# Kernel optimization log

Hardware: AMD Instinct MI355X
Metric: run time of the kernel (lower is better)

The kernel has to match this reference:

```python
import jax, jax.numpy as jnp
import numpy as np

# Config (mirrors CorrLayerDownsample(J=3, L=8, A=1, A_prime=1, M=256, N=256,
# num_channels=1, shift_mode='samec', mask_angles=4)). With samec + 1 channel,
# every pair is 'shifted' (mask index 1) and groups (j1,j2) are contiguous in
# the global moment order, so concatenation reproduces results_storage order.
J, L, A, M, N, NB = 3, 8, 1, 256, 256, 2
MASK_ANGLES = 4
RADII = (1, 2)  # dyadic shift radii (assumed form of create_masks_shift)

def _mask_positions():
    # shift mask 1: origin plus shifts along mask_angles directions at dyadic radii
    pos = {(0, 0)}
    for k in range(MASK_ANGLES):
        th = np.pi * k / MASK_ANGLES
        for r in RADII:
            pos.add((int(round(r * np.cos(th))), int(round(r * np.sin(th)))))
    return sorted(pos)

def _union_flat_idx(h, w):
    # row-major flat indices of the union shift mask at resolution (h, w),
    # matching torch boolean-mask indexing order (mask_downsample + mask_idx_map_1)
    return np.array(sorted(((dx % h) * w + (dy % w)) for dx, dy in _mask_positions()), dtype=np.int64)

UNION_IDX = [_union_flat_idx(M >> j, N >> j) for j in range(J)]
NSHIFT = len(UNION_IDX[0])

# per-(j1,j2) channel gather indices: la = A*L*c + A*l + a = l (A=1, c=0)
# loop order in compute_idx: l1 outer, l2 inner
LA1 = np.repeat(np.arange(L), L)
LA2 = np.tile(np.arange(L), L)

def _spectral_pad(xh, Mn, Nn):
    # zero-pad Fourier representation to (Mn, Nn) -- spectral upsampling
    m, n = xh.shape[-2], xh.shape[-1]
    if (m, n) == (Mn, Nn):
        return xh
    xs = jnp.fft.fftshift(xh, axes=(-2, -1))
    ph, pw = (Mn - m) // 2, (Nn - n) // 2
    pad = [(0, 0)] * (xh.ndim - 2) + [(ph, ph), (pw, pw)]
    xp = jnp.pad(xs, pad)
    return jnp.fft.ifftshift(xp, axes=(-2, -1)) * ((Mn * Nn) / (m * n))

def _forward(xpsi_0, xpsi_1, xpsi_2):
    xs = [xpsi_0, xpsi_1, xpsi_2]
    hats = [jnp.fft.fft2(x.astype(jnp.complex64)) for x in xs]  # [nb, C, h_j, w_j]
    la1 = jnp.asarray(LA1)
    la2 = jnp.asarray(LA2)
    outs = []
    for j1 in range(J):
        h, w = M >> j1, N >> j1
        uidx = jnp.asarray(UNION_IDX[j1])
        h1 = hats[j1][:, la1]  # [nb, P=L*L, h, w]
        for j2 in range(j1, J):
            h2 = hats[j2][:, la2]
            if j2 > j1:
                h2 = _spectral_pad(h2, h, w)  # upsample coarser scale to scale j1
            corr = jnp.fft.ifft2(h1 * jnp.conj(h2)).real  # cross-correlation map
            flat = corr.reshape(corr.shape[0], corr.shape[1], h * w)
            outs.append(flat[:, :, uidx])  # masked downsample: keep shift positions
    return jnp.concatenate(outs, axis=1)  # [nb, total_pairs, NSHIFT]

def setup_inputs():
    key = jax.random.key(0)
    ks = jax.random.split(key, 3)
    return {
        "xpsi_0": jax.random.normal(ks[0], (NB, A * L, M, N), dtype=jnp.float32),
        "xpsi_1": jax.random.normal(ks[1], (NB, A * L, M // 2, N // 2), dtype=jnp.float32),
        "xpsi_2": jax.random.normal(ks[2], (NB, A * L, M // 4, N // 4), dtype=jnp.float32),
    }

def reference(xpsi_0, xpsi_1, xpsi_2):
    return _forward(xpsi_0, xpsi_1, xpsi_2)
```

## Files before the change

### kernel.cpp

```cpp
#include <hip/hip_runtime.h>

#define PI_F 3.14159265358979323846f


__device__ __forceinline__ float rtab_f(int n, int m2, int t) {
  if (t == 0) return 1.0f;
  int tw = 2 * n - 1;
  float th = PI_F * (float)t / (float)n;
  int A = (t * (m2 - 1)) & tw;
  int B = (t * m2) & tw;
  float v = sinf(PI_F * (float)A / (float)n) / sinf(th) +
            cosf(PI_F * (float)B / (float)n);
  return v / (float)m2;
}

template <int NR>
__device__ __forceinline__ void phaseA256(const float* __restrict__ vch,
                                          const float* __restrict__ sRl,
                                          float* __restrict__ sh,
                                          const int (&rls)[NR], int mxg, int s,
                                          int n2, float inv, float Pv, float a,
                                          int per, int cid) {
  int bj[NR];
#pragma unroll
  for (int j = 0; j < NR; ++j) bj[j] = (mxg - 2 + rls[j]) & 255;
  float4 acc[NR];
#pragma unroll
  for (int j = 0; j < NR; ++j) acc[j] = make_float4(0.f, 0.f, 0.f, 0.f);
  const float4* vp = (const float4*)vch + cid;
  float4 va = vp[0];
  float4 vb = vp[64];
  for (int nx = 0; nx < n2; ++nx) {
    float4 vc = make_float4(0.f, 0.f, 0.f, 0.f);
    if (nx + 2 < n2) vc = vp[(size_t)(nx + 2) * 64];
    int ss = s * nx;
#pragma unroll
    for (int j = 0; j < NR; ++j) {
      float rv = sRl[(bj[j] - ss) & 255];
      acc[j].x += rv * va.x;
      acc[j].y += rv * va.y;
      acc[j].z += rv * va.z;
      acc[j].w += rv * va.w;
    }
    va = vb;
    vb = vc;
  }
  float smy[4];
#pragma unroll
  for (int j = 0; j < 4; ++j)
    smy[j] = sinf(a * (float)((4 * cid + j) & (per - 1)));
#pragma unroll
  for (int j = 0; j < NR; ++j) {
    float q = inv * sinf(a * (float)(bj[j] & (per - 1))) * Pv;
    float4 o = acc[j];
    o.x -= q * smy[0];
    o.y -= q * smy[1];
    o.z -= q * smy[2];
    o.w -= q * smy[3];
    *(float4*)&sh[rls[j] * 256 + 4 * cid] = o;
  }
}

template <int NR>
__device__ __forceinline__ void phaseA128(const float* __restrict__ vch,
                                          const float* __restrict__ sRl,
                                          float* __restrict__ sh,
                                          const int (&rls)[NR], int mxg, int n2,
                                          float inv, float Pv, int cid) {
  int bj[NR];
#pragma unroll
  for (int j = 0; j < NR; ++j) bj[j] = (mxg - 2 + rls[j]) & 127;
  float2 acc[NR];
#pragma unroll
  for (int j = 0; j < NR; ++j) acc[j] = make_float2(0.f, 0.f);
  const float2* vp = (const float2*)vch + cid;
  float2 va = vp[0];
  float2 vb = vp[64];
  for (int nx = 0; nx < n2; ++nx) {
    float2 vc = make_float2(0.f, 0.f);
    if (nx + 2 < n2) vc = vp[(size_t)(nx + 2) * 64];
    int ss = 2 * nx;
#pragma unroll
    for (int j = 0; j < NR; ++j) {
      float rv = sRl[(bj[j] - ss) & 127];
      acc[j].x += rv * va.x;
      acc[j].y += rv * va.y;
    }
    va = vb;
    vb = vc;
  }
  const float a = PI_F * 0.5f;
  float smy0 = sinf(a * (float)((2 * cid) & 3));
  float smy1 = sinf(a * (float)((2 * cid + 1) & 3));
#pragma unroll
  for (int j = 0; j < NR; ++j) {
    float q = inv * sinf(a * (float)(bj[j] & 3)) * Pv;
    float2 o = acc[j];
    o.x -= q * smy0;
    o.y -= q * smy1;
    *(float2*)&sh[rls[j] * 128 + 2 * cid] = o;
  }
}

__global__ __launch_bounds__(256) void k_front(
    const float* __restrict__ X0, const float* __restrict__ X1,
    const float* __restrict__ X2, float* __restrict__ P1p,
    float* __restrict__ P2p, float* __restrict__ V01, float* __restrict__ V02,
    float* __restrict__ V12, float* __restrict__ out) {
  __shared__ float fsm[4864];
  int bid = blockIdx.x;
  int t = threadIdx.x;
  if (bid < 192) {
    const float* X; float* P; int lg, nsp, idx0;
    if (bid < 128) { X = X1; P = P1p; lg = 7; nsp = 8; idx0 = bid; }
    else           { X = X2; P = P2p; lg = 6; nsp = 4; idx0 = bid - 128; }
    int ch = idx0 / nsp, split = idx0 % nsp;
    int n = 1 << lg;
    int total = n * n;
    int chunk = total / nsp;
    int b0 = split * chunk;
    const float* x = X + (size_t)ch * total + b0;
    float s = 0.f;
    for (int i = t; i < chunk; i += 256) {
      int idx = b0 + i;
      float v = x[i];
      s += (((idx >> lg) ^ idx) & 1) ? -v : v;
    }
#pragma unroll
    for (int off = 32; off > 0; off >>= 1) s += __shfl_down(s, off, 64);
    __shared__ float red[4];
    if ((t & 63) == 0) red[t >> 6] = s;
    __syncthreads();
    if (t == 0) P[ch * nsp + split] = red[0] + red[1] + red[2] + red[3];
    return;
  }
  if (bid < 320) {
    int idx = bid - 192;
    int ch = idx >> 3, nxg = (idx & 7) * 16;
    float* Rl = fsm;
    float* Xs = fsm + 256;
    for (int i = t; i < 256; i += 256) Rl[i] = rtab_f(256, 128, i);
    const float4* xch4 =
        (const float4*)(X1 + (size_t)ch * 16384 + (size_t)nxg * 128);
    for (int i = t; i < 512; i += 256) ((float4*)Xs)[i] = xch4[i];
    __syncthreads();
    float* vch = V01 + (size_t)ch * 128 * 256;
    for (int i = t; i < 2048; i += 256) {
      int r = i >> 7, k = i & 127;
      vch[(size_t)(nxg + r) * 256 + 2 * k] = Xs[r * 128 + k];
    }
    int cid = t & 63, wq = t >> 6;
    int m0 = 2 * cid + 1, m1 = 2 * cid + 129;
    float acc[4][2];
#pragma unroll
    for (int r = 0; r < 4; ++r) { acc[r][0] = 0.f; acc[r][1] = 0.f; }
    for (int ny = 0; ny < 128; ++ny) {
      float r0 = Rl[(m0 - 2 * ny) & 255];
      float r1 = Rl[(m1 - 2 * ny) & 255];
#pragma unroll
      for (int r = 0; r < 4; ++r) {
        float xv = Xs[(4 * wq + r) * 128 + ny];
        acc[r][0] += xv * r0;
        acc[r][1] += xv * r1;
      }
    }
#pragma unroll
    for (int r = 0; r < 4; ++r) {
      vch[(size_t)(nxg + 4 * wq + r) * 256 + m0] = acc[r][0];
      vch[(size_t)(nxg + 4 * wq + r) * 256 + m1] = acc[r][1];
    }
    return;
  }
  if (bid < 512) {
    int vbid = bid - 320;
    const float* X = X2; float* V;
    int n1, n2, s, ch, nxg, colh;
    if (vbid < 128) {
      V = V02; n1 = 256; n2 = 64; s = 4;
      ch = vbid >> 3; nxg = ((vbid >> 1) & 3) * 16; colh = vbid & 1;
    } else {
      int w = vbid - 128;
      V = V12; n1 = 128; n2 = 64; s = 2;
      ch = w >> 2; nxg = (w & 3) * 16; colh = 0;
    }
    float* Rl = fsm;
    float* Xs = fsm + 256;
    for (int i = t; i < n1; i += 256) Rl[i] = rtab_f(n1, n2, i);
    const float4* xch4 =
        (const float4*)(X + (size_t)ch * n2 * n2 + (size_t)nxg * n2);
    int nx4 = (16 * n2) >> 2;
    for (int i = t; i < nx4; i += 256) ((float4*)Xs)[i] = xch4[i];
    __syncthreads();
    int myq = (t & 63) + colh * 128;
    int nxq = t >> 6;
    int mask = n1 - 1;
    float acc[4][2];
#pragma unroll
    for (int r = 0; r < 4; ++r)
#pragma unroll
      for (int c = 0; c < 2; ++c) acc[r][c] = 0.f;
    for (int ny = 0; ny < n2; ++ny) {
      float xv[4];
#pragma unroll
      for (int r = 0; r < 4; ++r) xv[r] = Xs[(4 * nxq + r) * n2 + ny];
#pragma unroll
      for (int c = 0; c < 2; ++c) {
        float rv = Rl[(myq + 64 * c - s * ny) & mask];
#pragma unroll
        for (int r = 0; r < 4; ++r) acc[r][c] += xv[r] * rv;
      }
    }
    float* vch = V + (size_t)ch * n2 * n1;
#pragma unroll
    for (int r = 0; r < 4; ++r)
      for (int c = 0; c < 2; ++c)
        vch[(size_t)(nxg + 4 * nxq + r) * n1 + myq + 64 * c] = acc[r][c];
    return;
  }
  int lane = t & 63;
  int wv = t >> 6;
  float accC[8][7];
#pragma unroll
  for (int i = 0; i < 8; ++i)
#pragma unroll
    for (int p = 0; p < 7; ++p) accC[i][p] = 0.f;
  int w = bid - 512;
  const float* Ab; int loc, lgn1, lgc, base;
  if (w < 256)      { loc = w;       Ab = X0; lgn1 = 8; lgc = 4; base = 0;   }
  else if (w < 384) { loc = w - 256; Ab = X1; lgn1 = 7; lgc = 3; base = 192; }
  else              { loc = w - 384; Ab = X2; lgn1 = 6; lgc = 2; base = 320; }
  int n1 = 1 << lgn1;
  int mask = n1 - 1;
  int n1sq = n1 * n1;
  int chunk = loc & ((1 << lgc) - 1);
  int bl2 = loc >> lgc;
  int b = bl2 >> 3, l2 = bl2 & 7;
  const float* A1 = Ab + (size_t)(b * 8) * n1sq;
  const float* A2 = Ab + (size_t)(b * 8 + l2) * n1sq;
  int lgtpr = lgn1 - 2;
  int tpr = 1 << lgtpr;
  int rif = 256 >> lgtpr;
  int rid = t >> lgtpr;
  int cid2 = t & (tpr - 1);
  int ty = cid2 * 4;
  int tym = (ty - 4) & mask;
  for (int rr = 0; rr < 16; rr += rif) {
    int row = chunk * 16 + rr + rid;
    const float* r0 = A2 + (size_t)row * n1;
    const float* r1 = A2 + (size_t)((row - 1) & mask) * n1;
    const float* r2 = A2 + (size_t)((row - 2) & mask) * n1;
    const float* r3 = A2 + (size_t)((row + 1) & mask) * n1;
    float4 a0 = *(const float4*)(r0 + tym);
    float4 b0 = *(const float4*)(r0 + ty);
    float4 a1 = *(const float4*)(r1 + tym);
    float4 b1 = *(const float4*)(r1 + ty);
    float4 b2 = *(const float4*)(r2 + ty);
    float4 a3 = *(const float4*)(r3 + tym);
    float4 b3 = *(const float4*)(r3 + ty);
    const float* rA = A1 + (size_t)row * n1 + ty;
#pragma unroll
    for (int l1 = 0; l1 < 8; ++l1) {
      float4 xv = *(const float4*)(rA + (size_t)l1 * n1sq);
      accC[l1][0] += xv.x * b0.x + xv.y * b0.y + xv.z * b0.z + xv.w * b0.w;
      accC[l1][1] += xv.x * a0.w + xv.y * b0.x + xv.z * b0.y + xv.w * b0.z;
      accC[l1][2] += xv.x * a0.z + xv.y * a0.w + xv.z * b0.x + xv.w * b0.y;
      accC[l1][3] += xv.x * b1.x + xv.y * b1.y + xv.z * b1.z + xv.w * b1.w;
      accC[l1][4] += xv.x * a1.w + xv.y * b1.x + xv.z * b1.y + xv.w * b1.z;
      accC[l1][5] += xv.x * b2.x + xv.y * b2.y + xv.z * b2.z + xv.w * b2.w;
      accC[l1][6] += xv.x * a3.w + xv.y * b3.x + xv.z * b3.y + xv.w * b3.z;
    }
  }
  float* sh = fsm;
  float* af = &accC[0][0];
#pragma unroll
  for (int j = 0; j < 56; ++j) {
    float v = af[j];
    v += __shfl_down(v, 32, 64);
    v += __shfl_down(v, 16, 64);
    af[j] = v;
  }
  __syncthreads();
  if (lane < 16) {
    float* rowp = sh + (wv * 16 + lane) * 60;
#pragma unroll
    for (int j = 0; j < 14; ++j)
      *(float4*)&rowp[4 * j] =
          make_float4(af[4 * j], af[4 * j + 1], af[4 * j + 2], af[4 * j + 3]);
  }
  __syncthreads();
  if (t < 224) {
    int v = t >> 2, q = t & 3;
    float s2 = 0.f;
#pragma unroll
    for (int i = 0; i < 16; ++i) s2 += sh[(q * 16 + i) * 60 + v];
    s2 += __shfl_down(s2, 2, 64);
    s2 += __shfl_down(s2, 1, 64);
    if (q == 0) {
      int l1o = v / 7, p = v % 7;
      atomicAdd(&out[((size_t)b * 384 + base + l1o * 8 + l2) * 7 + p], s2);
    }
  }
}

__global__ __launch_bounds__(256) void k_main(const float* __restrict__ X0,
                                              const float* __restrict__ X1,
                                              const float* __restrict__ V01,
                                              const float* __restrict__ V02,
                                              const float* __restrict__ V12,
                                              const float* __restrict__ P1p,
                                              const float* __restrict__ P2p,
                                              float* __restrict__ out) {
  __shared__ float sRl[256];
  __shared__ float sh[4864];
  int u = blockIdx.x;
  int t = threadIdx.x;
  int lane = t & 63;
  int wv = t >> 6;

  float accC[8][7];
#pragma unroll
  for (int i = 0; i < 8; ++i)
#pragma unroll
    for (int p = 0; p < 7; ++p) accC[i][p] = 0.f;

  const float* V; const float* Pp; const float* A1b;
  int n1, n2, s, ch, chunk, nsp, lgn1, base; float inv;
  if (u < 256) {
    V = V01; Pp = P1p; nsp = 8; A1b = X0; n1 = 256; n2 = 128; s = 2;
    inv = 1.f / 16384.f; ch = u >> 4; chunk = u & 15; lgn1 = 8; base = 64;
  } else if (u < 512) {
    int w = u - 256;
    V = V02; Pp = P2p; nsp = 4; A1b = X0; n1 = 256; n2 = 64; s = 4;
    inv = 1.f / 4096.f; ch = w >> 4; chunk = w & 15; lgn1 = 8; base = 128;
  } else {
    int w = u - 512;
    V = V12; Pp = P2p; nsp = 4; A1b = X1; n1 = 128; n2 = 64; s = 2;
    inv = 1.f / 4096.f; ch = w >> 3; chunk = w & 7; lgn1 = 7; base = 256;
  }
  int mask = n1 - 1;
  for (int i = t; i < n1; i += 256) sRl[i] = rtab_f(n1, n2, i);
  __syncthreads();
  int mxg = chunk * 16;
  int b = ch >> 3, l2 = ch & 7;
  const float* vch = V + (size_t)ch * n2 * n1;
  float Pv = 0.f;
  for (int i = 0; i < nsp; ++i) Pv += Pp[ch * nsp + i];
  float a = PI_F / (float)s;
  int per = 2 * s;

  if (n1 == 256) {
    if (s == 2) {
      if (wv < 3) {
        int rls[3] = {6 * wv + 1, 6 * wv + 3, 6 * wv + 5};
        phaseA256<3>(vch, sRl, sh, rls, mxg, 2, 128, inv, Pv, a, per, lane);
      } else {
        for (int i = lane; i < 640; i += 64) {
          int rl = 2 * (i >> 6), c4 = (i & 63) * 4;
          int mx = (mxg - 2 + rl) & 255;
          *(float4*)&sh[rl * 256 + c4] =
              *(const float4*)(vch + (size_t)(mx >> 1) * 256 + c4);
        }
      }
    } else {
      if (wv == 0) {
        int rls[4] = {0, 1, 3, 4};
        phaseA256<4>(vch, sRl, sh, rls, mxg, 4, 64, inv, Pv, a, per, lane);
      } else if (wv == 1) {
        int rls[4] = {5, 7, 8, 9};
        phaseA256<4>(vch, sRl, sh, rls, mxg, 4, 64, inv, Pv, a, per, lane);
      } else if (wv == 2) {
        int rls[3] = {11, 12, 13};
        phaseA256<3>(vch, sRl, sh, rls, mxg, 4, 64, inv, Pv, a, per, lane);
      } else {
        int rls[3] = {15, 16, 17};
        phaseA256<3>(vch, sRl, sh, rls, mxg, 4, 64, inv, Pv, a, per, lane);
      }
      for (int i = t; i < 320; i += 256) {
        int rl = 2 + 4 * (i >> 6), c4 = (i & 63) * 4;
        int mx = (mxg - 2 + rl) & 255;
        *(float4*)&sh[rl * 256 + c4] =
            *(const float4*)(vch + (size_t)(mx >> 2) * 256 + c4);
      }
    }
  } else {
    if (wv < 3) {
      int rls[3] = {6 * wv + 1, 6 * wv + 3, 6 * wv + 5};
      phaseA128<3>(vch, sRl, sh, rls, mxg, 64, inv, Pv, lane);
    } else {
      for (int i = lane; i < 320; i += 64) {
        int rl = 2 * (i >> 5), c4 = (i & 31) * 4;
        int mx = (mxg - 2 + rl) & 127;
        *(float4*)&sh[rl * 128 + c4] =
            *(const float4*)(vch + (size_t)(mx >> 1) * 128 + c4);
      }
    }
  }
  __syncthreads();

  int lgtpr = lgn1 - 2;
  int tpr = 1 << lgtpr;
  int rif = 256 >> lgtpr;
  int rid = t >> lgtpr;
  int cid2 = t & (tpr - 1);
  int ty = cid2 * 4;
  int tym = (ty - 4) & mask;
  int n1sq = n1 * n1;
  const float* A1 = A1b + (size_t)(b * 8) * n1sq;
  for (int rr = 0; rr < 16; rr += rif) {
    int ri = rr + rid;
    const float* r0 = &sh[(ri + 2) * n1];
    const float* r1 = &sh[(ri + 1) * n1];
    const float* r2 = &sh[ri * n1];
    const float* r3 = &sh[(ri + 3) * n1];
    float4 a0 = *(const float4*)(r0 + tym);
    float4 b0 = *(const float4*)(r0 + ty);
    float4 a1 = *(const float4*)(r1 + tym);
    float4 b1 = *(const float4*)(r1 + ty);
    float4 b2 = *(const float4*)(r2 + ty);
    float4 a3 = *(const float4*)(r3 + tym);
    float4 b3 = *(const float4*)(r3 + ty);
    const float* rA = A1 + (size_t)(mxg + ri) * n1 + ty;
#pragma unroll
    for (int l1 = 0; l1 < 8; ++l1) {
      float4 xv = *(const float4*)(rA + (size_t)l1 * n1sq);
      accC[l1][0] += xv.x * b0.x + xv.y * b0.y + xv.z * b0.z + xv.w * b0.w;
      accC[l1][1] += xv.x * a0.w + xv.y * b0.x + xv.z * b0.y + xv.w * b0.z;
      accC[l1][2] += xv.x * a0.z + xv.y * a0.w + xv.z * b0.x + xv.w * b0.y;
      accC[l1][3] += xv.x * b1.x + xv.y * b1.y + xv.z * b1.z + xv.w * b1.w;
      accC[l1][4] += xv.x * a1.w + xv.y * b1.x + xv.z * b1.y + xv.w * b1.z;
      accC[l1][5] += xv.x * b2.x + xv.y * b2.y + xv.z * b2.z + xv.w * b2.w;
      accC[l1][6] += xv.x * a3.w + xv.y * b3.x + xv.z * b3.y + xv.w * b3.z;
    }
  }

  float* af = &accC[0][0];
#pragma unroll
  for (int j = 0; j < 56; ++j) {
    float v = af[j];
    v += __shfl_down(v, 32, 64);
    v += __shfl_down(v, 16, 64);
    af[j] = v;
  }
  __syncthreads();
  if (lane < 16) {
    float* rowp = sh + (wv * 16 + lane) * 60;
#pragma unroll
    for (int j = 0; j < 14; ++j)
      *(float4*)&rowp[4 * j] =
          make_float4(af[4 * j], af[4 * j + 1], af[4 * j + 2], af[4 * j + 3]);
  }
  __syncthreads();
  if (t < 224) {
    int v = t >> 2, q = t & 3;
    float s2 = 0.f;
#pragma unroll
    for (int i = 0; i < 16; ++i) s2 += sh[(q * 16 + i) * 60 + v];
    s2 += __shfl_down(s2, 2, 64);
    s2 += __shfl_down(s2, 1, 64);
    if (q == 0) {
      int l1o = v / 7, p = v % 7;
      atomicAdd(&out[((size_t)b * 384 + base + l1o * 8 + l2) * 7 + p], s2);
    }
  }
}

extern "C" void kernel_launch(void* const* d_in, const int* in_sizes, int n_in,
                              void* d_out, int out_size, void* d_ws, size_t ws_size,
                              hipStream_t stream) {
  const float* X0 = (const float*)d_in[0];
  const float* X1 = (const float*)d_in[1];
  const float* X2 = (const float*)d_in[2];
  float* out = (float*)d_out;
  float* ws = (float*)d_ws;

  float* V01 = ws + 2359296;
  float* V02 = ws + 2883584;
  float* V12 = ws + 3145728;
  float* P1p = ws + 3276800;
  float* P2p = ws + 3276928;

  hipMemsetAsync(d_out, 0, (size_t)out_size, stream);
  k_front<<<960, 256, 0, stream>>>(X0, X1, X2, P1p, P2p, V01, V02, V12, out);
  k_main<<<640, 256, 0, stream>>>(X0, X1, V01, V02, V12, P1p, P2p, out);
}
```

Before: 96.56 us.

## Split row chunks across twice as many blocks and precompute interpolation tables once

Both kernels now split each 16-row chunk into two 8-row halves, doubling the grid so more blocks run in parallel and each block needs a smaller shared-memory halo. The resampling table is computed in double precision in the front kernel, written to workspace, and loaded by the main kernel instead of being recomputed with transcendental calls in every block. The front kernel also reorders its block roles so the heavy correlation blocks come first. In exchange, the halo rows overlapping each chunk are rebuilt twice, and the per-block phase-A work is split unevenly across waves.

```diff
diff --git a/kernel.cpp b/kernel.cpp
--- a/kernel.cpp
+++ b/kernel.cpp
@@ -1,17 +1,14 @@
 #include <hip/hip_runtime.h>
 
+#define PI_D 3.14159265358979323846
 #define PI_F 3.14159265358979323846f
 
 
-__device__ __forceinline__ float rtab_f(int n, int m2, int t) {
+__device__ inline float rtab_val(int n, int m2, int t) {
   if (t == 0) return 1.0f;
-  int tw = 2 * n - 1;
-  float th = PI_F * (float)t / (float)n;
-  int A = (t * (m2 - 1)) & tw;
-  int B = (t * m2) & tw;
-  float v = sinf(PI_F * (float)A / (float)n) / sinf(th) +
-            cosf(PI_F * (float)B / (float)n);
-  return v / (float)m2;
+  double th = PI_D * (double)t / (double)n;
+  double v = sin(th * (double)(m2 - 1)) / sin(th) + cos(th * (double)m2);
+  return (float)(v / (double)m2);
 }
 
 template <int NR>
@@ -106,14 +103,16 @@
     const float* __restrict__ X0, const float* __restrict__ X1,
     const float* __restrict__ X2, float* __restrict__ P1p,
     float* __restrict__ P2p, float* __restrict__ V01, float* __restrict__ V02,
-    float* __restrict__ V12, float* __restrict__ out) {
-  __shared__ float fsm[4864];
+    float* __restrict__ V12, float* __restrict__ T01, float* __restrict__ T02,
+    float* __restrict__ T12, float* __restrict__ out) {
+  __shared__ float fsm[3840];
   int bid = blockIdx.x;
   int t = threadIdx.x;
-  if (bid < 192) {
+  if (bid >= 1152) {
+    int pb = bid - 1152;
     const float* X; float* P; int lg, nsp, idx0;
-    if (bid < 128) { X = X1; P = P1p; lg = 7; nsp = 8; idx0 = bid; }
-    else           { X = X2; P = P2p; lg = 6; nsp = 4; idx0 = bid - 128; }
+    if (pb < 128) { X = X1; P = P1p; lg = 7; nsp = 8; idx0 = pb; }
+    else          { X = X2; P = P2p; lg = 6; nsp = 4; idx0 = pb - 128; }
     int ch = idx0 / nsp, split = idx0 % nsp;
     int n = 1 << lg;
     int total = n * n;
@@ -134,16 +133,18 @@
     if (t == 0) P[ch * nsp + split] = red[0] + red[1] + red[2] + red[3];
     return;
   }
-  if (bid < 320) {
-    int idx = bid - 192;
+  if (bid >= 768 && bid < 896) {
+    int idx = bid - 768;
     int ch = idx >> 3, nxg = (idx & 7) * 16;
     float* Rl = fsm;
     float* Xs = fsm + 256;
-    for (int i = t; i < 256; i += 256) Rl[i] = rtab_f(256, 128, i);
+    for (int i = t; i < 256; i += 256) Rl[i] = rtab_val(256, 128, i);
     const float4* xch4 =
         (const float4*)(X1 + (size_t)ch * 16384 + (size_t)nxg * 128);
     for (int i = t; i < 512; i += 256) ((float4*)Xs)[i] = xch4[i];
     __syncthreads();
+    if (idx == 0)
+      for (int i = t; i < 256; i += 256) T01[i] = Rl[i];
     float* vch = V01 + (size_t)ch * 128 * 256;
     for (int i = t; i < 2048; i += 256) {
       int r = i >> 7, k = i & 127;
@@ -171,8 +172,8 @@
     }
     return;
   }
-  if (bid < 512) {
-    int vbid = bid - 320;
+  if (bid >= 896 && bid < 1088) {
+    int vbid = bid - 896;
     const float* X = X2; float* V;
     int n1, n2, s, ch, nxg, colh;
     if (vbid < 128) {
@@ -185,12 +186,16 @@
     }
     float* Rl = fsm;
     float* Xs = fsm + 256;
-    for (int i = t; i < n1; i += 256) Rl[i] = rtab_f(n1, n2, i);
+    for (int i = t; i < n1; i += 256) Rl[i] = rtab_val(n1, n2, i);
     const float4* xch4 =
         (const float4*)(X + (size_t)ch * n2 * n2 + (size_t)nxg * n2);
     int nx4 = (16 * n2) >> 2;
     for (int i = t; i < nx4; i += 256) ((float4*)Xs)[i] = xch4[i];
     __syncthreads();
+    if (vbid == 0)
+      for (int i = t; i < 256; i += 256) T02[i] = Rl[i];
+    if (vbid == 128)
+      for (int i = t; i < 128; i += 256) T12[i] = Rl[i];
     int myq = (t & 63) + colh * 128;
     int nxq = t >> 6;
     int mask = n1 - 1;
@@ -224,11 +229,18 @@
   for (int i = 0; i < 8; ++i)
 #pragma unroll
     for (int p = 0; p < 7; ++p) accC[i][p] = 0.f;
-  int w = bid - 512;
-  const float* Ab; int loc, lgn1, lgc, base;
-  if (w < 256)      { loc = w;       Ab = X0; lgn1 = 8; lgc = 4; base = 0;   }
-  else if (w < 384) { loc = w - 256; Ab = X1; lgn1 = 7; lgc = 3; base = 192; }
-  else              { loc = w - 384; Ab = X2; lgn1 = 6; lgc = 2; base = 320; }
+  const float* Ab; int loc, half, lgn1, lgc, base, nrows;
+  if (bid < 512) {
+    loc = bid >> 1; half = bid & 1; Ab = X0; lgn1 = 8; lgc = 4; base = 0;
+    nrows = 8;
+  } else if (bid < 768) {
+    int q = bid - 512;
+    loc = q >> 1; half = q & 1; Ab = X1; lgn1 = 7; lgc = 3; base = 192;
+    nrows = 8;
+  } else {
+    loc = bid - 1088; half = 0; Ab = X2; lgn1 = 6; lgc = 2; base = 320;
+    nrows = 16;
+  }
   int n1 = 1 << lgn1;
   int mask = n1 - 1;
   int n1sq = n1 * n1;
@@ -244,8 +256,9 @@
   int cid2 = t & (tpr - 1);
   int ty = cid2 * 4;
   int tym = (ty - 4) & mask;
-  for (int rr = 0; rr < 16; rr += rif) {
-    int row = chunk * 16 + rr + rid;
+  int row0 = chunk * 16 + half * 8;
+  for (int rr = 0; rr < nrows; rr += rif) {
+    int row = row0 + rr + rid;
     const float* r0 = A2 + (size_t)row * n1;
     const float* r1 = A2 + (size_t)((row - 1) & mask) * n1;
     const float* r2 = A2 + (size_t)((row - 2) & mask) * n1;
@@ -309,10 +322,15 @@
                                               const float* __restrict__ V12,
                                               const float* __restrict__ P1p,
                                               const float* __restrict__ P2p,
+                                              const float* __restrict__ T01,
+                                              const float* __restrict__ T02,
+                                              const float* __restrict__ T12,
                                               float* __restrict__ out) {
   __shared__ float sRl[256];
-  __shared__ float sh[4864];
-  int u = blockIdx.x;
+  __shared__ float sh[3840];
+  int up = blockIdx.x;
+  int u = up >> 1;
+  int half = up & 1;
   int t = threadIdx.x;
   int lane = t & 63;
   int wv = t >> 6;
@@ -323,24 +341,27 @@
 #pragma unroll
     for (int p = 0; p < 7; ++p) accC[i][p] = 0.f;
 
-  const float* V; const float* Pp; const float* A1b;
+  const float* V; const float* Pp; const float* A1b; const float* T;
   int n1, n2, s, ch, chunk, nsp, lgn1, base; float inv;
   if (u < 256) {
     V = V01; Pp = P1p; nsp = 8; A1b = X0; n1 = 256; n2 = 128; s = 2;
     inv = 1.f / 16384.f; ch = u >> 4; chunk = u & 15; lgn1 = 8; base = 64;
+    T = T01;
   } else if (u < 512) {
     int w = u - 256;
     V = V02; Pp = P2p; nsp = 4; A1b = X0; n1 = 256; n2 = 64; s = 4;
     inv = 1.f / 4096.f; ch = w >> 4; chunk = w & 15; lgn1 = 8; base = 128;
+    T = T02;
   } else {
     int w = u - 512;
     V = V12; Pp = P2p; nsp = 4; A1b = X1; n1 = 128; n2 = 64; s = 2;
     inv = 1.f / 4096.f; ch = w >> 3; chunk = w & 7; lgn1 = 7; base = 256;
+    T = T12;
   }
   int mask = n1 - 1;
-  for (int i = t; i < n1; i += 256) sRl[i] = rtab_f(n1, n2, i);
+  for (int i = t; i < n1; i += 256) sRl[i] = T[i];
   __syncthreads();
-  int mxg = chunk * 16;
+  int mxg = chunk * 16 + half * 8;
   int b = ch >> 3, l2 = ch & 7;
   const float* vch = V + (size_t)ch * n2 * n1;
   float Pv = 0.f;
@@ -350,11 +371,17 @@
 
   if (n1 == 256) {
     if (s == 2) {
-      if (wv < 3) {
-        int rls[3] = {6 * wv + 1, 6 * wv + 3, 6 * wv + 5};
-        phaseA256<3>(vch, sRl, sh, rls, mxg, 2, 128, inv, Pv, a, per, lane);
+      if (wv == 0) {
+        int rls[2] = {1, 3};
+        phaseA256<2>(vch, sRl, sh, rls, mxg, 2, 128, inv, Pv, a, per, lane);
+      } else if (wv == 1) {
+        int rls[2] = {5, 7};
+        phaseA256<2>(vch, sRl, sh, rls, mxg, 2, 128, inv, Pv, a, per, lane);
+      } else if (wv == 2) {
+        int rls[1] = {9};
+        phaseA256<1>(vch, sRl, sh, rls, mxg, 2, 128, inv, Pv, a, per, lane);
       } else {
-        for (int i = lane; i < 640; i += 64) {
+        for (int i = lane; i < 384; i += 64) {
           int rl = 2 * (i >> 6), c4 = (i & 63) * 4;
           int mx = (mxg - 2 + rl) & 255;
           *(float4*)&sh[rl * 256 + c4] =
@@ -363,19 +390,19 @@
       }
     } else {
       if (wv == 0) {
-        int rls[4] = {0, 1, 3, 4};
-        phaseA256<4>(vch, sRl, sh, rls, mxg, 4, 64, inv, Pv, a, per, lane);
+        int rls[2] = {0, 1};
+        phaseA256<2>(vch, sRl, sh, rls, mxg, 4, 64, inv, Pv, a, per, lane);
       } else if (wv == 1) {
-        int rls[4] = {5, 7, 8, 9};
-        phaseA256<4>(vch, sRl, sh, rls, mxg, 4, 64, inv, Pv, a, per, lane);
+        int rls[2] = {3, 4};
+        phaseA256<2>(vch, sRl, sh, rls, mxg, 4, 64, inv, Pv, a, per, lane);
       } else if (wv == 2) {
-        int rls[3] = {11, 12, 13};
-        phaseA256<3>(vch, sRl, sh, rls, mxg, 4, 64, inv, Pv, a, per, lane);
+        int rls[2] = {5, 7};
+        phaseA256<2>(vch, sRl, sh, rls, mxg, 4, 64, inv, Pv, a, per, lane);
       } else {
-        int rls[3] = {15, 16, 17};
-        phaseA256<3>(vch, sRl, sh, rls, mxg, 4, 64, inv, Pv, a, per, lane);
+        int rls[2] = {8, 9};
+        phaseA256<2>(vch, sRl, sh, rls, mxg, 4, 64, inv, Pv, a, per, lane);
       }
-      for (int i = t; i < 320; i += 256) {
+      for (int i = t; i < 192; i += 256) {
         int rl = 2 + 4 * (i >> 6), c4 = (i & 63) * 4;
         int mx = (mxg - 2 + rl) & 255;
         *(float4*)&sh[rl * 256 + c4] =
@@ -383,11 +410,17 @@
       }
     }
   } else {
-    if (wv < 3) {
-      int rls[3] = {6 * wv + 1, 6 * wv + 3, 6 * wv + 5};
-      phaseA128<3>(vch, sRl, sh, rls, mxg, 64, inv, Pv, lane);
+    if (wv == 0) {
+      int rls[2] = {1, 3};
+      phaseA128<2>(vch, sRl, sh, rls, mxg, 64, inv, Pv, lane);
+    } else if (wv == 1) {
+      int rls[2] = {5, 7};
+      phaseA128<2>(vch, sRl, sh, rls, mxg, 64, inv, Pv, lane);
+    } else if (wv == 2) {
+      int rls[1] = {9};
+      phaseA128<1>(vch, sRl, sh, rls, mxg, 64, inv, Pv, lane);
     } else {
-      for (int i = lane; i < 320; i += 64) {
+      for (int i = lane; i < 192; i += 64) {
         int rl = 2 * (i >> 5), c4 = (i & 31) * 4;
         int mx = (mxg - 2 + rl) & 127;
         *(float4*)&sh[rl * 128 + c4] =
@@ -406,7 +439,7 @@
   int tym = (ty - 4) & mask;
   int n1sq = n1 * n1;
   const float* A1 = A1b + (size_t)(b * 8) * n1sq;
-  for (int rr = 0; rr < 16; rr += rif) {
+  for (int rr = 0; rr < 8; rr += rif) {
     int ri = rr + rid;
     const float* r0 = &sh[(ri + 2) * n1];
     const float* r1 = &sh[(ri + 1) * n1];
@@ -478,8 +511,13 @@
   float* V12 = ws + 3145728;
   float* P1p = ws + 3276800;
   float* P2p = ws + 3276928;
+  float* T01 = ws + 3276992;
+  float* T02 = ws + 3277248;
+  float* T12 = ws + 3277504;
 
   hipMemsetAsync(d_out, 0, (size_t)out_size, stream);
-  k_front<<<960, 256, 0, stream>>>(X0, X1, X2, P1p, P2p, V01, V02, V12, out);
-  k_main<<<640, 256, 0, stream>>>(X0, X1, V01, V02, V12, P1p, P2p, out);
+  k_front<<<1344, 256, 0, stream>>>(X0, X1, X2, P1p, P2p, V01, V02, V12, T01,
+                                    T02, T12, out);
+  k_main<<<1280, 256, 0, stream>>>(X0, X1, V01, V02, V12, P1p, P2p, T01, T02,
+                                   T12, out);
 }
```

Measured after the change: 145.2 us. 1.5x slower.

## Precompute rtab tables once in front kernel, batch-prefetch V rows in phaseA

Applied to the files above, without the earlier changes.

The resampling table is now computed in double precision in k_front and written to workspace (T01/T02/T12), and k_main loads it instead of recomputing trig per block. The phaseA inner loops switch from a two-deep rolling prefetch to loading eight rows at a time into registers, aiming to raise memory-level parallelism. k_front's shared memory shrinks. The trade-offs are double-precision trig in the front kernel, higher register pressure from the 8-wide buffers, and a loop that assumes n2 is a multiple of 8.

```diff
diff --git a/kernel.cpp b/kernel.cpp
--- a/kernel.cpp
+++ b/kernel.cpp
@@ -1,17 +1,14 @@
 #include <hip/hip_runtime.h>
 
+#define PI_D 3.14159265358979323846
 #define PI_F 3.14159265358979323846f
 
 
-__device__ __forceinline__ float rtab_f(int n, int m2, int t) {
+__device__ inline float rtab_val(int n, int m2, int t) {
   if (t == 0) return 1.0f;
-  int tw = 2 * n - 1;
-  float th = PI_F * (float)t / (float)n;
-  int A = (t * (m2 - 1)) & tw;
-  int B = (t * m2) & tw;
-  float v = sinf(PI_F * (float)A / (float)n) / sinf(th) +
-            cosf(PI_F * (float)B / (float)n);
-  return v / (float)m2;
+  double th = PI_D * (double)t / (double)n;
+  double v = sin(th * (double)(m2 - 1)) / sin(th) + cos(th * (double)m2);
+  return (float)(v / (double)m2);
 }
 
 template <int NR>
@@ -28,22 +25,28 @@
 #pragma unroll
   for (int j = 0; j < NR; ++j) acc[j] = make_float4(0.f, 0.f, 0.f, 0.f);
   const float4* vp = (const float4*)vch + cid;
-  float4 va = vp[0];
-  float4 vb = vp[64];
-  for (int nx = 0; nx < n2; ++nx) {
-    float4 vc = make_float4(0.f, 0.f, 0.f, 0.f);
-    if (nx + 2 < n2) vc = vp[(size_t)(nx + 2) * 64];
-    int ss = s * nx;
-#pragma unroll
-    for (int j = 0; j < NR; ++j) {
-      float rv = sRl[(bj[j] - ss) & 255];
-      acc[j].x += rv * va.x;
-      acc[j].y += rv * va.y;
-      acc[j].z += rv * va.z;
-      acc[j].w += rv * va.w;
-    }
-    va = vb;
-    vb = vc;
+  float4 cur[8], nxt[8];
+#pragma unroll
+  for (int k = 0; k < 8; ++k) cur[k] = vp[(size_t)k * 64];
+  for (int nx = 0; nx < n2; nx += 8) {
+    if (nx + 8 < n2) {
+#pragma unroll
+      for (int k = 0; k < 8; ++k) nxt[k] = vp[(size_t)(nx + 8 + k) * 64];
+    }
+#pragma unroll
+    for (int k = 0; k < 8; ++k) {
+      int ss = s * (nx + k);
+#pragma unroll
+      for (int j = 0; j < NR; ++j) {
+        float rv = sRl[(bj[j] - ss) & 255];
+        acc[j].x += rv * cur[k].x;
+        acc[j].y += rv * cur[k].y;
+        acc[j].z += rv * cur[k].z;
+        acc[j].w += rv * cur[k].w;
+      }
+    }
+#pragma unroll
+    for (int k = 0; k < 8; ++k) cur[k] = nxt[k];
   }
   float smy[4];
 #pragma unroll
@@ -74,20 +77,26 @@
 #pragma unroll
   for (int j = 0; j < NR; ++j) acc[j] = make_float2(0.f, 0.f);
   const float2* vp = (const float2*)vch + cid;
-  float2 va = vp[0];
-  float2 vb = vp[64];
-  for (int nx = 0; nx < n2; ++nx) {
-    float2 vc = make_float2(0.f, 0.f);
-    if (nx + 2 < n2) vc = vp[(size_t)(nx + 2) * 64];
-    int ss = 2 * nx;
-#pragma unroll
-    for (int j = 0; j < NR; ++j) {
-      float rv = sRl[(bj[j] - ss) & 127];
-      acc[j].x += rv * va.x;
-      acc[j].y += rv * va.y;
-    }
-    va = vb;
-    vb = vc;
+  float2 cur[8], nxt[8];
+#pragma unroll
+  for (int k = 0; k < 8; ++k) cur[k] = vp[(size_t)k * 64];
+  for (int nx = 0; nx < n2; nx += 8) {
+    if (nx + 8 < n2) {
+#pragma unroll
+      for (int k = 0; k < 8; ++k) nxt[k] = vp[(size_t)(nx + 8 + k) * 64];
+    }
+#pragma unroll
+    for (int k = 0; k < 8; ++k) {
+      int ss = 2 * (nx + k);
+#pragma unroll
+      for (int j = 0; j < NR; ++j) {
+        float rv = sRl[(bj[j] - ss) & 127];
+        acc[j].x += rv * cur[k].x;
+        acc[j].y += rv * cur[k].y;
+      }
+    }
+#pragma unroll
+    for (int k = 0; k < 8; ++k) cur[k] = nxt[k];
   }
   const float a = PI_F * 0.5f;
   float smy0 = sinf(a * (float)((2 * cid) & 3));
@@ -106,8 +115,9 @@
     const float* __restrict__ X0, const float* __restrict__ X1,
     const float* __restrict__ X2, float* __restrict__ P1p,
     float* __restrict__ P2p, float* __restrict__ V01, float* __restrict__ V02,
-    float* __restrict__ V12, float* __restrict__ out) {
-  __shared__ float fsm[4864];
+    float* __restrict__ V12, float* __restrict__ T01, float* __restrict__ T02,
+    float* __restrict__ T12, float* __restrict__ out) {
+  __shared__ float fsm[3840];
   int bid = blockIdx.x;
   int t = threadIdx.x;
   if (bid < 192) {
@@ -139,11 +149,13 @@
     int ch = idx >> 3, nxg = (idx & 7) * 16;
     float* Rl = fsm;
     float* Xs = fsm + 256;
-    for (int i = t; i < 256; i += 256) Rl[i] = rtab_f(256, 128, i);
+    for (int i = t; i < 256; i += 256) Rl[i] = rtab_val(256, 128, i);
     const float4* xch4 =
         (const float4*)(X1 + (size_t)ch * 16384 + (size_t)nxg * 128);
     for (int i = t; i < 512; i += 256) ((float4*)Xs)[i] = xch4[i];
     __syncthreads();
+    if (idx == 0)
+      for (int i = t; i < 256; i += 256) T01[i] = Rl[i];
     float* vch = V01 + (size_t)ch * 128 * 256;
     for (int i = t; i < 2048; i += 256) {
       int r = i >> 7, k = i & 127;
@@ -185,12 +197,16 @@
     }
     float* Rl = fsm;
     float* Xs = fsm + 256;
-    for (int i = t; i < n1; i += 256) Rl[i] = rtab_f(n1, n2, i);
+    for (int i = t; i < n1; i += 256) Rl[i] = rtab_val(n1, n2, i);
     const float4* xch4 =
         (const float4*)(X + (size_t)ch * n2 * n2 + (size_t)nxg * n2);
     int nx4 = (16 * n2) >> 2;
     for (int i = t; i < nx4; i += 256) ((float4*)Xs)[i] = xch4[i];
     __syncthreads();
+    if (vbid == 0)
+      for (int i = t; i < 256; i += 256) T02[i] = Rl[i];
+    if (vbid == 128)
+      for (int i = t; i < 128; i += 256) T12[i] = Rl[i];
     int myq = (t & 63) + colh * 128;
     int nxq = t >> 6;
     int mask = n1 - 1;
@@ -309,6 +325,9 @@
                                               const float* __restrict__ V12,
                                               const float* __restrict__ P1p,
                                               const float* __restrict__ P2p,
+                                              const float* __restrict__ T01,
+                                              const float* __restrict__ T02,
+                                              const float* __restrict__ T12,
                                               float* __restrict__ out) {
   __shared__ float sRl[256];
   __shared__ float sh[4864];
@@ -323,22 +342,25 @@
 #pragma unroll
     for (int p = 0; p < 7; ++p) accC[i][p] = 0.f;
 
-  const float* V; const float* Pp; const float* A1b;
+  const float* V; const float* Pp; const float* A1b; const float* T;
   int n1, n2, s, ch, chunk, nsp, lgn1, base; float inv;
   if (u < 256) {
     V = V01; Pp = P1p; nsp = 8; A1b = X0; n1 = 256; n2 = 128; s = 2;
     inv = 1.f / 16384.f; ch = u >> 4; chunk = u & 15; lgn1 = 8; base = 64;
+    T = T01;
   } else if (u < 512) {
     int w = u - 256;
     V = V02; Pp = P2p; nsp = 4; A1b = X0; n1 = 256; n2 = 64; s = 4;
     inv = 1.f / 4096.f; ch = w >> 4; chunk = w & 15; lgn1 = 8; base = 128;
+    T = T02;
   } else {
     int w = u - 512;
     V = V12; Pp = P2p; nsp = 4; A1b = X1; n1 = 128; n2 = 64; s = 2;
     inv = 1.f / 4096.f; ch = w >> 3; chunk = w & 7; lgn1 = 7; base = 256;
+    T = T12;
   }
   int mask = n1 - 1;
-  for (int i = t; i < n1; i += 256) sRl[i] = rtab_f(n1, n2, i);
+  for (int i = t; i < n1; i += 256) sRl[i] = T[i];
   __syncthreads();
   int mxg = chunk * 16;
   int b = ch >> 3, l2 = ch & 7;
@@ -478,8 +500,13 @@
   float* V12 = ws + 3145728;
   float* P1p = ws + 3276800;
   float* P2p = ws + 3276928;
+  float* T01 = ws + 3276992;
+  float* T02 = ws + 3277248;
+  float* T12 = ws + 3277504;
 
   hipMemsetAsync(d_out, 0, (size_t)out_size, stream);
-  k_front<<<960, 256, 0, stream>>>(X0, X1, X2, P1p, P2p, V01, V02, V12, out);
-  k_main<<<640, 256, 0, stream>>>(X0, X1, V01, V02, V12, P1p, P2p, out);
+  k_front<<<960, 256, 0, stream>>>(X0, X1, X2, P1p, P2p, V01, V02, V12, T01,
+                                   T02, T12, out);
+  k_main<<<640, 256, 0, stream>>>(X0, X1, V01, V02, V12, P1p, P2p, T01, T02,
+                                  T12, out);
 }
```

Measured after the change: 114.3 us. 1.18x slower.
